# Optimization experiments

Measured on AMD Instinct MI355X. Metric: run time of the kernel, lower is better.

## Reference

```python
import jax, jax.numpy as jnp
import numpy as np

NUM_CLASSES = 2
LOG2_NC = float(np.log2(NUM_CLASSES))


def _conv(x, w, b=None):
    # NCHW conv, stride 1, SAME padding (kernel 3 pad 1 or kernel 1 pad 0)
    y = jax.lax.conv_general_dilated(x, w, (1, 1), 'SAME',
                                     dimension_numbers=('NCHW', 'OIHW', 'NCHW'))
    if b is not None:
        y = y + b[None, :, None, None]
    return y


def _uncertainty_map(ds):
    # entropy over class dim, thresholded to {0,1}
    logp = jax.nn.log_softmax(ds, axis=1)            # [B,C,H,W]
    prob = jnp.exp(logp)
    # torch uses log2(prob + 1e-6); replicate exactly
    ent = -jnp.sum(prob * jnp.log2(prob + 1e-6), axis=1) / LOG2_NC  # [B,H,W]
    return (ent >= 0.001).astype(jnp.float32)


def _unob(tar, amap):
    # vectorized UnoB with S=3: interior pixels with tar!=0 get pro=0 unless
    # 4*tar == sum of the 4-neighborhood (i.e. locally constant label)
    t = tar  # [B,H,W] int
    nb = t[:, 2:, 1:-1] + t[:, :-2, 1:-1] + t[:, 1:-1, 2:] + t[:, 1:-1, :-2]
    center = t[:, 1:-1, 1:-1]
    inner_pro = jnp.where((center != 0) & (4 * center != nb), 0.0, 1.0)
    pro = jnp.ones_like(amap)
    pro = pro.at[:, 1:-1, 1:-1].set(inner_pro)
    return amap * pro


def setup_inputs() -> dict:
    key = jax.random.key(0)
    ks = jax.random.split(key, 6)
    B, C, H, W = 8, 128, 128, 128
    return {
        'x': jax.random.normal(ks[0], (B, C, H, W), jnp.float32),
        'skip': jax.random.normal(ks[1], (B, C, H, W), jnp.float32),
        'tar': jax.random.randint(ks[2], (B, 1, H, W), 0, NUM_CLASSES, jnp.int64)
            if jax.config.jax_enable_x64 else
            jax.random.randint(ks[2], (B, 1, H, W), 0, NUM_CLASSES).astype(jnp.int32),
        'W1': jax.random.normal(ks[3], (128, 256, 3, 3), jnp.float32) * 0.05,
        'b1': jnp.zeros((128,), jnp.float32),
        'W2': jax.random.normal(ks[4], (128, 128, 3, 3), jnp.float32) * 0.05,
        'b2': jnp.zeros((128,), jnp.float32),
        'Wds': jax.random.normal(ks[5], (NUM_CLASSES, 128, 1, 1), jnp.float32) * 0.05,
    }


def reference(x, skip, tar, W1, b1, W2, b2, Wds):
    h = jnp.concatenate([x, skip], axis=1)            # [B,2*dim,H,W]
    h = jax.nn.leaky_relu(_conv(h, W1, b1), 0.01)     # [B,dim,H,W]
    h = jax.nn.leaky_relu(_conv(h, W2, b2), 0.01)
    ds = _conv(h, Wds)                                # [B,num_classes,H,W]
    amap = _uncertainty_map(ds)                       # [B,H,W]
    amap = _unob(tar[:, 0], amap)                     # UnoB refinement, S=3
    return h, ds, amap
```

## Files before the change

### kernel.cpp

```cpp
#include <hip/hip_runtime.h>

typedef float f32x16 __attribute__((ext_vector_type(16)));
typedef short bf16x8 __attribute__((ext_vector_type(8)));
typedef unsigned int u32;

static __device__ __forceinline__ unsigned short f2bf(float f) {
  union { float f; unsigned int u; } v;
  v.f = f;
  return (unsigned short)((v.u + 0x7FFFu + ((v.u >> 16) & 1u)) >> 16);
}

static __device__ __forceinline__ void gl_lds16(const unsigned short* g,
                                                unsigned short* l) {
  __builtin_amdgcn_global_load_lds(
      (const __attribute__((address_space(1))) u32*)g,
      (__attribute__((address_space(3))) u32*)l, 16, 0, 0);
}

#define VMCNT4 asm volatile("s_waitcnt vmcnt(4)" ::: "memory")
#define VMCNT0 asm volatile("s_waitcnt vmcnt(0)" ::: "memory")
#define LGKM0 asm volatile("s_waitcnt lgkmcnt(0)" ::: "memory")
#define BAR __builtin_amdgcn_s_barrier()
#define SCHEDB __builtin_amdgcn_sched_barrier(0)

__global__ __launch_bounds__(256) void convert_weights(
    const float* __restrict__ W1, const float* __restrict__ W2,
    unsigned short* __restrict__ W1b, unsigned short* __restrict__ W2b,
    unsigned short* __restrict__ zp) {
  if (blockIdx.x == 1728) {
    uint4* z = (uint4*)zp;
    z[threadIdx.x] = make_uint4(0, 0, 0, 0);
    z[256 + threadIdx.x] = make_uint4(0, 0, 0, 0);
    return;
  }
  int i = blockIdx.x * 256 + threadIdx.x;
  if (i < 294912) {
    int e = i & 7, co = (i >> 3) & 127, r = i >> 10;
    int tap = r % 9, pc = r / 9;
    int ci = (pc >> 1) * 16 + (pc & 1) * 8 + e;
    W1b[i] = f2bf(W1[(co * 256 + ci) * 9 + tap]);
  } else {
    int j = i - 294912;
    if (j < 147456) {
      int e = j & 7, co = (j >> 3) & 127, r = j >> 10;
      int tap = r % 9, pc = r / 9;
      int ci = (pc >> 1) * 16 + (pc & 1) * 8 + e;
      W2b[j] = f2bf(W2[(co * 128 + ci) * 9 + tap]);
    }
  }
}

__global__ __launch_bounds__(256) void transpose_to_bf16(
    const float* __restrict__ x, const float* __restrict__ skip,
    unsigned short* __restrict__ dst) {
  int bid = blockIdx.x;
  const float* src = (bid < 1024) ? x : skip;
  int cigb = (bid < 1024) ? 0 : 16;
  int row = bid & 1023;
  int b = row >> 7, y = row & 127;
  const float* s = src + (long)b * 128 * 16384 + (long)y * 128;
  for (int it = 0; it < 8; ++it) {
    int u = it * 256 + (int)threadIdx.x;
    int cig = u >> 7, px = u & 127;
    unsigned short pk[8];
#pragma unroll
    for (int e = 0; e < 8; ++e)
      pk[e] = f2bf(s[(long)(cig * 8 + e) * 16384 + px]);
    uint4 vv;
    vv.x = (unsigned)pk[0] | ((unsigned)pk[1] << 16);
    vv.y = (unsigned)pk[2] | ((unsigned)pk[3] << 16);
    vv.z = (unsigned)pk[4] | ((unsigned)pk[5] << 16);
    vv.w = (unsigned)pk[6] | ((unsigned)pk[7] << 16);
    *(uint4*)(&dst[(((long)row * 32 + cigb + cig) * 130 + px + 1) * 8]) = vv;
  }
  if (cigb == 0 && threadIdx.x < 64) {
    int g = threadIdx.x >> 1;
    long col = (threadIdx.x & 1) * 129L;
    *(uint4*)(&dst[(((long)row * 32 + g) * 130 + col) * 8]) = make_uint4(0, 0, 0, 0);
  }
}

template <int CIN, bool FUSE_DS>
__global__ __launch_bounds__(256, 2) void conv3x3(
    const unsigned short* __restrict__ src,
    const unsigned short* __restrict__ wt,
    const float* __restrict__ bias,
    const unsigned short* __restrict__ zp,
    unsigned short* __restrict__ dst_bf16,
    float* __restrict__ dst_f32,
    const float* __restrict__ wds,
    const int* __restrict__ tar,
    float* __restrict__ ds,
    float* __restrict__ amap) {
  constexpr int CPG = CIN / 8;
  constexpr int NC = CIN / 16;
  __shared__ unsigned short in_tile[2][1040 * 8];
  __shared__ float sb[128];
  __shared__ float w0s[128], w1s[128];
  __shared__ float sc[2 * 4 * 2 * 32];

  const int tid = threadIdx.x;
  const int wg = (blockIdx.x & 7) * 64 + (blockIdx.x >> 3);
  const int b = wg >> 6;
  const int y0 = (wg & 63) * 2;
  const int lane = tid & 63, wave = tid >> 6;
  const int wco = wave & 1, wrow = wave >> 1;
  const int l31 = lane & 31, kh = lane >> 5;

  if (tid < 128) {
    sb[tid] = bias[tid];
    if constexpr (FUSE_DS) {
      w0s[tid] = wds[tid];
      w1s[tid] = wds[128 + tid];
    }
  }

#define STAGE_IN(cic, bufi)                                                    \
  {                                                                            \
    _Pragma("unroll") for (int j = 0; j < 4; ++j) {                            \
      int o = wave * 4 + j;                                                    \
      int s = o * 64 + lane;                                                   \
      int p = s >= 520;                                                        \
      int r = s - p * 520;                                                     \
      int hy = r / 130;                                                        \
      int hx = r - hy * 130;                                                   \
      int gy = y0 - 1 + hy;                                                    \
      const unsigned short* g =                                                \
          (gy >= 0 && gy < 128)                                                \
              ? src + ((size_t)((b * 128 + gy) * CPG) + (size_t)(cic)*2 + p) * \
                          1040 +                                               \
                    hx * 8                                                     \
              : zp + lane * 8;                                                 \
      gl_lds16(g, &in_tile[bufi][(size_t)o * 512]);                            \
    }                                                                          \
  }

#define LOAD_TAIL(cic, v)                                                      \
  {                                                                            \
    if (tid < 16) {                                                            \
      int gy_ = y0 + 2;                                                        \
      if (gy_ < 128)                                                           \
        v = *(const uint4*)(src +                                              \
                            ((size_t)((b * 128 + gy_) * CPG) +                 \
                             (size_t)(cic)*2 + 1) *                            \
                                1040 +                                         \
                            (114 + tid) * 8);                                  \
    }                                                                          \
  }

#define WRITE_TAIL(bufi, v)                                                    \
  {                                                                            \
    if (tid < 16) *(uint4*)(&in_tile[bufi][(size_t)(1024 + tid) * 8]) = v;     \
  }

  f32x16 acc[2][4] = {};

  const unsigned short* wlane =
      wt + (size_t)kh * 9216 + (size_t)(wco * 64 + l31) * 8;

  {
    uint4 tv = make_uint4(0, 0, 0, 0);
    LOAD_TAIL(0, tv);
    STAGE_IN(0, 0);
    VMCNT0;
    WRITE_TAIL(0, tv);
    LGKM0;
    BAR;
    SCHEDB;
  }
  bf16x8 a0[3], a1[3];
#pragma unroll
  for (int t = 0; t < 3; ++t) {
    a0[t] = *(const bf16x8*)(wlane + t * 1024);
    a1[t] = *(const bf16x8*)(wlane + t * 1024 + 256);
  }

  for (int cic = 0; cic < NC; ++cic) {
    const int cur = cic & 1, nbuf = cur ^ 1;
    const bool more = (cic + 1 < NC);
    uint4 tl = make_uint4(0, 0, 0, 0);
    SCHEDB;
    if (more) {
      LOAD_TAIL(cic + 1, tl);
      STAGE_IN(cic + 1, nbuf);
      SCHEDB;
      VMCNT4;
      SCHEDB;
      WRITE_TAIL(nbuf, tl);
    } else {
      VMCNT0;
    }
    LGKM0;
    BAR;
    SCHEDB;

    const unsigned short* wl = wlane + (size_t)cic * 18432;
    const unsigned short* wlnext = wlane + (size_t)(more ? cic + 1 : cic) * 18432;
    const unsigned short* it = &in_tile[cur][0];
    const size_t ib = (size_t)kh * 4160;
#pragma unroll
    for (int ky = 0; ky < 3; ++ky) {
      const int hy = ky + wrow;
      bf16x8 n0[3], n1[3];
      if (ky < 2) {
#pragma unroll
        for (int t = 0; t < 3; ++t) {
          n0[t] = *(const bf16x8*)(wl + (ky * 3 + 3 + t) * 1024);
          n1[t] = *(const bf16x8*)(wl + (ky * 3 + 3 + t) * 1024 + 256);
        }
      } else {
#pragma unroll
        for (int t = 0; t < 3; ++t) {
          n0[t] = *(const bf16x8*)(wlnext + t * 1024);
          n1[t] = *(const bf16x8*)(wlnext + t * 1024 + 256);
        }
      }
#pragma unroll
      for (int kx = 0; kx < 3; ++kx) {
        bf16x8 b0 = *(const bf16x8*)(&it[ib + (size_t)(hy * 130 + l31 + kx) * 8]);
        bf16x8 b1 = *(const bf16x8*)(&it[ib + (size_t)(hy * 130 + 32 + l31 + kx) * 8]);
        bf16x8 b2 = *(const bf16x8*)(&it[ib + (size_t)(hy * 130 + 64 + l31 + kx) * 8]);
        bf16x8 b3 = *(const bf16x8*)(&it[ib + (size_t)(hy * 130 + 96 + l31 + kx) * 8]);
        acc[0][0] = __builtin_amdgcn_mfma_f32_32x32x16_bf16(a0[kx], b0, acc[0][0], 0, 0, 0);
        acc[0][1] = __builtin_amdgcn_mfma_f32_32x32x16_bf16(a0[kx], b1, acc[0][1], 0, 0, 0);
        acc[0][2] = __builtin_amdgcn_mfma_f32_32x32x16_bf16(a0[kx], b2, acc[0][2], 0, 0, 0);
        acc[0][3] = __builtin_amdgcn_mfma_f32_32x32x16_bf16(a0[kx], b3, acc[0][3], 0, 0, 0);
        acc[1][0] = __builtin_amdgcn_mfma_f32_32x32x16_bf16(a1[kx], b0, acc[1][0], 0, 0, 0);
        acc[1][1] = __builtin_amdgcn_mfma_f32_32x32x16_bf16(a1[kx], b1, acc[1][1], 0, 0, 0);
        acc[1][2] = __builtin_amdgcn_mfma_f32_32x32x16_bf16(a1[kx], b2, acc[1][2], 0, 0, 0);
        acc[1][3] = __builtin_amdgcn_mfma_f32_32x32x16_bf16(a1[kx], b3, acc[1][3], 0, 0, 0);
      }
#pragma unroll
      for (int t = 0; t < 3; ++t) { a0[t] = n0[t]; a1[t] = n1[t]; }
    }
    SCHEDB;
    LGKM0;
    BAR;
    SCHEDB;
  }

  const int gyo = y0 + wrow;
  float pd[4][2] = {};
#pragma unroll
  for (int fc = 0; fc < 2; ++fc) {
#pragma unroll
    for (int fp = 0; fp < 4; ++fp) {
      const int px = fp * 32 + l31;
      if constexpr (!FUSE_DS) {
#pragma unroll
        for (int rg = 0; rg < 4; ++rg) {
          const int co0 = wco * 64 + fc * 32 + rg * 8 + kh * 4;
          unsigned short pk[4];
#pragma unroll
          for (int q = 0; q < 4; ++q) {
            float v = acc[fc][fp][rg * 4 + q] + sb[co0 + q];
            v = v > 0.f ? v : 0.01f * v;
            pk[q] = f2bf(v);
          }
          uint2 o;
          o.x = (unsigned)pk[0] | ((unsigned)pk[1] << 16);
          o.y = (unsigned)pk[2] | ((unsigned)pk[3] << 16);
          *(uint2*)(&dst_bf16[(((long)(b * 128 + gyo) * 16 + (co0 >> 3)) * 130 + px + 1) * 8 +
                              kh * 4]) = o;
        }
      } else {
#pragma unroll
        for (int rg = 0; rg < 4; ++rg) {
          const int co0 = wco * 64 + fc * 32 + rg * 8 + kh * 4;
          float4 wv0 = *(const float4*)(&w0s[co0]);
          float4 wv1 = *(const float4*)(&w1s[co0]);
#pragma unroll
          for (int q = 0; q < 4; ++q) {
            float v = acc[fc][fp][rg * 4 + q] + sb[co0 + q];
            v = v > 0.f ? v : 0.01f * v;
            dst_f32[((long)(b * 128 + co0 + q) << 14) + (gyo << 7) + px] = v;
            float wq0 = (q == 0) ? wv0.x : (q == 1) ? wv0.y : (q == 2) ? wv0.z : wv0.w;
            float wq1 = (q == 0) ? wv1.x : (q == 1) ? wv1.y : (q == 2) ? wv1.z : wv1.w;
            pd[fp][0] += wq0 * v;
            pd[fp][1] += wq1 * v;
          }
        }
      }
    }
  }

  if constexpr (!FUSE_DS) {
    if (tid < 64) {
      int row = tid >> 5, g = (tid >> 1) & 15;
      long col = (tid & 1) * 129L;
      *(uint4*)(&dst_bf16[(((long)(b * 128 + y0 + row) * 16 + g) * 130 + col) * 8]) =
          make_uint4(0, 0, 0, 0);
    }
  } else {
#pragma unroll
    for (int fp = 0; fp < 4; ++fp)
#pragma unroll
      for (int c = 0; c < 2; ++c)
        pd[fp][c] += __shfl_xor(pd[fp][c], 32, 64);
    if (wco == 1 && kh == 0) {
#pragma unroll
      for (int fp = 0; fp < 4; ++fp)
#pragma unroll
        for (int c = 0; c < 2; ++c)
          sc[((wrow * 4 + fp) * 2 + c) * 32 + l31] = pd[fp][c];
    }
    __syncthreads();
    if (wco == 0 && kh == 0) {
      const int* tb = tar + (long)b * 16384;
#pragma unroll
      for (int fp = 0; fp < 4; ++fp) {
        const int px = fp * 32 + l31;
        float a0f = pd[fp][0] + sc[((wrow * 4 + fp) * 2 + 0) * 32 + l31];
        float a1f = pd[fp][1] + sc[((wrow * 4 + fp) * 2 + 1) * 32 + l31];
        ds[((long)b * 2) * 16384 + (gyo << 7) + px] = a0f;
        ds[((long)b * 2 + 1) * 16384 + (gyo << 7) + px] = a1f;
        float m = fmaxf(a0f, a1f);
        float e0 = expf(a0f - m), e1 = expf(a1f - m);
        float s = e0 + e1;
        float p0f = e0 / s, p1f = e1 / s;
        float ent = -(p0f * log2f(p0f + 1e-6f) + p1f * log2f(p1f + 1e-6f));
        float un = ent >= 0.001f ? 1.f : 0.f;
        float pro = 1.f;
        if (gyo > 0 && gyo < 127 && px > 0 && px < 127) {
          int c = tb[(gyo << 7) + px];
          if (c != 0) {
            int nb2 = tb[((gyo - 1) << 7) + px] + tb[((gyo + 1) << 7) + px] +
                      tb[(gyo << 7) + px - 1] + tb[(gyo << 7) + px + 1];
            if (4 * c != nb2) pro = 0.f;
          }
        }
        amap[((long)(b * 128 + gyo) << 7) + px] = un * pro;
      }
    }
  }
#undef STAGE_IN
#undef LOAD_TAIL
#undef WRITE_TAIL
}

extern "C" void kernel_launch(void* const* d_in, const int* in_sizes, int n_in,
                              void* d_out, int out_size, void* d_ws, size_t ws_size,
                              hipStream_t stream) {
  const float* x    = (const float*)d_in[0];
  const float* skip = (const float*)d_in[1];
  const int*   tar  = (const int*)d_in[2];
  const float* W1   = (const float*)d_in[3];
  const float* b1   = (const float*)d_in[4];
  const float* W2   = (const float*)d_in[5];
  const float* b2   = (const float*)d_in[6];
  const float* Wds  = (const float*)d_in[7];

  float* out_h  = (float*)d_out;
  float* out_ds = out_h + 16777216;
  float* out_am = out_ds + 262144;

  unsigned short* W1b = (unsigned short*)d_ws;
  unsigned short* W2b = W1b + 294912;
  unsigned short* zp  = W2b + 147456;
  unsigned short* h1  = (unsigned short*)((char*)d_ws + (1u << 20));

  unsigned short* h0 = (unsigned short*)d_out;

  convert_weights<<<1729, 256, 0, stream>>>(W1, W2, W1b, W2b, zp);
  transpose_to_bf16<<<2048, 256, 0, stream>>>(x, skip, h0);
  conv3x3<256, false><<<512, 256, 0, stream>>>(h0, W1b, b1, zp, h1, nullptr,
                                               nullptr, nullptr, nullptr, nullptr);
  conv3x3<128, true><<<512, 256, 0, stream>>>(h1, W2b, b2, zp, nullptr, out_h,
                                              Wds, tar, out_ds, out_am);
}
```

Measured before the change: 151.1 us.

## Split conv3x3 work across 8 waves per block with padded LDS rows

Doubles the block size to 512 threads so each wave computes half the pixel columns (2 MFMA tiles per row instead of 4), cutting accumulator registers and raising waves per CU. The LDS input tile row stride is padded to 136, and staging is simplified to precomputed global pointers with per-wave load counts, removing the separate tail load path. Weight register prefetching across ky/channel chunks is dropped in favour of loading weights right before use, which trades fewer registers for possibly more exposed global-load latency.

After: 178.3 us. 18.0% more time.

```diff
diff --git a/kernel.cpp b/kernel.cpp
--- a/kernel.cpp
+++ b/kernel.cpp
@@ -17,7 +17,8 @@
       (__attribute__((address_space(3))) u32*)l, 16, 0, 0);
 }
 
-#define VMCNT4 asm volatile("s_waitcnt vmcnt(4)" ::: "memory")
+#define VMCNT3 asm volatile("s_waitcnt vmcnt(3)" ::: "memory")
+#define VMCNT2 asm volatile("s_waitcnt vmcnt(2)" ::: "memory")
 #define VMCNT0 asm volatile("s_waitcnt vmcnt(0)" ::: "memory")
 #define LGKM0 asm volatile("s_waitcnt lgkmcnt(0)" ::: "memory")
 #define BAR __builtin_amdgcn_s_barrier()
@@ -81,7 +82,7 @@
 }
 
 template <int CIN, bool FUSE_DS>
-__global__ __launch_bounds__(256, 2) void conv3x3(
+__global__ __launch_bounds__(512, 4) void conv3x3(
     const unsigned short* __restrict__ src,
     const unsigned short* __restrict__ wt,
     const float* __restrict__ bias,
@@ -94,17 +95,17 @@
     float* __restrict__ amap) {
   constexpr int CPG = CIN / 8;
   constexpr int NC = CIN / 16;
-  __shared__ unsigned short in_tile[2][1040 * 8];
+  __shared__ unsigned short in_tile[2][1088 * 8];
   __shared__ float sb[128];
   __shared__ float w0s[128], w1s[128];
-  __shared__ float sc[2 * 4 * 2 * 32];
+  __shared__ float sc[2 * 2 * 2 * 2 * 32];
 
   const int tid = threadIdx.x;
   const int wg = (blockIdx.x & 7) * 64 + (blockIdx.x >> 3);
   const int b = wg >> 6;
   const int y0 = (wg & 63) * 2;
   const int lane = tid & 63, wave = tid >> 6;
-  const int wco = wave & 1, wrow = wave >> 1;
+  const int wco = wave & 1, wpx = (wave >> 1) & 1, wrow = wave >> 2;
   const int l31 = lane & 31, kh = lane >> 5;
 
   if (tid < 128) {
@@ -115,123 +116,76 @@
     }
   }
 
-#define STAGE_IN(cic, bufi)                                                    \
-  {                                                                            \
-    _Pragma("unroll") for (int j = 0; j < 4; ++j) {                            \
-      int o = wave * 4 + j;                                                    \
-      int s = o * 64 + lane;                                                   \
-      int p = s >= 520;                                                        \
-      int r = s - p * 520;                                                     \
-      int hy = r / 130;                                                        \
-      int hx = r - hy * 130;                                                   \
-      int gy = y0 - 1 + hy;                                                    \
-      const unsigned short* g =                                                \
-          (gy >= 0 && gy < 128)                                                \
-              ? src + ((size_t)((b * 128 + gy) * CPG) + (size_t)(cic)*2 + p) * \
-                          1040 +                                               \
-                    hx * 8                                                     \
-              : zp + lane * 8;                                                 \
-      gl_lds16(g, &in_tile[bufi][(size_t)o * 512]);                            \
-    }                                                                          \
-  }
-
-#define LOAD_TAIL(cic, v)                                                      \
-  {                                                                            \
-    if (tid < 16) {                                                            \
-      int gy_ = y0 + 2;                                                        \
-      if (gy_ < 128)                                                           \
-        v = *(const uint4*)(src +                                              \
-                            ((size_t)((b * 128 + gy_) * CPG) +                 \
-                             (size_t)(cic)*2 + 1) *                            \
-                                1040 +                                         \
-                            (114 + tid) * 8);                                  \
-    }                                                                          \
-  }
-
-#define WRITE_TAIL(bufi, v)                                                    \
-  {                                                                            \
-    if (tid < 16) *(uint4*)(&in_tile[bufi][(size_t)(1024 + tid) * 8]) = v;     \
-  }
-
-  f32x16 acc[2][4] = {};
+  const int nops = (wave == 0) ? 3 : 2;
+  const unsigned short* gbase[3];
+  int gstr[3];
+  int lofs[3];
+#pragma unroll
+  for (int i = 0; i < 3; ++i) {
+    const int o = (i < 2) ? (wave * 2 + i) : 16;
+    const int s = o * 64 + lane;
+    const int p = s >= 544;
+    const int r = s - p * 544;
+    const int hy = r / 136;
+    const int hx = r - hy * 136;
+    const int gy = y0 - 1 + hy;
+    const bool ok = (hx < 130) && (gy >= 0) && (gy < 128);
+    gbase[i] = ok ? src + ((size_t)((b * 128 + gy) * CPG) + p) * 1040 + hx * 8
+                  : zp + lane * 8;
+    gstr[i] = ok ? 2080 : 0;
+    lofs[i] = o * 512;
+  }
+
+  f32x16 acc[2][2] = {};
+
+#pragma unroll
+  for (int i = 0; i < 3; ++i)
+    if (i < nops) gl_lds16(gbase[i], &in_tile[0][(size_t)lofs[i]]);
+  VMCNT0;
+  BAR;
 
   const unsigned short* wlane =
       wt + (size_t)kh * 9216 + (size_t)(wco * 64 + l31) * 8;
-
-  {
-    uint4 tv = make_uint4(0, 0, 0, 0);
-    LOAD_TAIL(0, tv);
-    STAGE_IN(0, 0);
-    VMCNT0;
-    WRITE_TAIL(0, tv);
-    LGKM0;
-    BAR;
-    SCHEDB;
-  }
-  bf16x8 a0[3], a1[3];
-#pragma unroll
-  for (int t = 0; t < 3; ++t) {
-    a0[t] = *(const bf16x8*)(wlane + t * 1024);
-    a1[t] = *(const bf16x8*)(wlane + t * 1024 + 256);
-  }
 
   for (int cic = 0; cic < NC; ++cic) {
     const int cur = cic & 1, nbuf = cur ^ 1;
     const bool more = (cic + 1 < NC);
-    uint4 tl = make_uint4(0, 0, 0, 0);
-    SCHEDB;
     if (more) {
-      LOAD_TAIL(cic + 1, tl);
-      STAGE_IN(cic + 1, nbuf);
+#pragma unroll
+      for (int i = 0; i < 3; ++i)
+        if (i < nops)
+          gl_lds16(gbase[i] + (size_t)(cic + 1) * gstr[i],
+                   &in_tile[nbuf][(size_t)lofs[i]]);
       SCHEDB;
-      VMCNT4;
-      SCHEDB;
-      WRITE_TAIL(nbuf, tl);
+      if (wave == 0) { VMCNT3; } else { VMCNT2; }
     } else {
       VMCNT0;
     }
-    LGKM0;
+    SCHEDB;
     BAR;
     SCHEDB;
 
     const unsigned short* wl = wlane + (size_t)cic * 18432;
-    const unsigned short* wlnext = wlane + (size_t)(more ? cic + 1 : cic) * 18432;
     const unsigned short* it = &in_tile[cur][0];
-    const size_t ib = (size_t)kh * 4160;
+    const size_t ib = (size_t)kh * (544 * 8);
 #pragma unroll
     for (int ky = 0; ky < 3; ++ky) {
       const int hy = ky + wrow;
-      bf16x8 n0[3], n1[3];
-      if (ky < 2) {
-#pragma unroll
-        for (int t = 0; t < 3; ++t) {
-          n0[t] = *(const bf16x8*)(wl + (ky * 3 + 3 + t) * 1024);
-          n1[t] = *(const bf16x8*)(wl + (ky * 3 + 3 + t) * 1024 + 256);
-        }
-      } else {
-#pragma unroll
-        for (int t = 0; t < 3; ++t) {
-          n0[t] = *(const bf16x8*)(wlnext + t * 1024);
-          n1[t] = *(const bf16x8*)(wlnext + t * 1024 + 256);
-        }
+      bf16x8 a0[3], a1[3];
+#pragma unroll
+      for (int t = 0; t < 3; ++t) {
+        a0[t] = *(const bf16x8*)(wl + (ky * 3 + t) * 1024);
+        a1[t] = *(const bf16x8*)(wl + (ky * 3 + t) * 1024 + 256);
       }
 #pragma unroll
       for (int kx = 0; kx < 3; ++kx) {
-        bf16x8 b0 = *(const bf16x8*)(&it[ib + (size_t)(hy * 130 + l31 + kx) * 8]);
-        bf16x8 b1 = *(const bf16x8*)(&it[ib + (size_t)(hy * 130 + 32 + l31 + kx) * 8]);
-        bf16x8 b2 = *(const bf16x8*)(&it[ib + (size_t)(hy * 130 + 64 + l31 + kx) * 8]);
-        bf16x8 b3 = *(const bf16x8*)(&it[ib + (size_t)(hy * 130 + 96 + l31 + kx) * 8]);
+        bf16x8 b0 = *(const bf16x8*)(&it[ib + (size_t)(hy * 136 + wpx * 64 + l31 + kx) * 8]);
+        bf16x8 b1 = *(const bf16x8*)(&it[ib + (size_t)(hy * 136 + wpx * 64 + 32 + l31 + kx) * 8]);
         acc[0][0] = __builtin_amdgcn_mfma_f32_32x32x16_bf16(a0[kx], b0, acc[0][0], 0, 0, 0);
         acc[0][1] = __builtin_amdgcn_mfma_f32_32x32x16_bf16(a0[kx], b1, acc[0][1], 0, 0, 0);
-        acc[0][2] = __builtin_amdgcn_mfma_f32_32x32x16_bf16(a0[kx], b2, acc[0][2], 0, 0, 0);
-        acc[0][3] = __builtin_amdgcn_mfma_f32_32x32x16_bf16(a0[kx], b3, acc[0][3], 0, 0, 0);
         acc[1][0] = __builtin_amdgcn_mfma_f32_32x32x16_bf16(a1[kx], b0, acc[1][0], 0, 0, 0);
         acc[1][1] = __builtin_amdgcn_mfma_f32_32x32x16_bf16(a1[kx], b1, acc[1][1], 0, 0, 0);
-        acc[1][2] = __builtin_amdgcn_mfma_f32_32x32x16_bf16(a1[kx], b2, acc[1][2], 0, 0, 0);
-        acc[1][3] = __builtin_amdgcn_mfma_f32_32x32x16_bf16(a1[kx], b3, acc[1][3], 0, 0, 0);
       }
-#pragma unroll
-      for (int t = 0; t < 3; ++t) { a0[t] = n0[t]; a1[t] = n1[t]; }
     }
     SCHEDB;
     LGKM0;
@@ -240,12 +194,12 @@
   }
 
   const int gyo = y0 + wrow;
-  float pd[4][2] = {};
+  float pd[2][2] = {};
 #pragma unroll
   for (int fc = 0; fc < 2; ++fc) {
 #pragma unroll
-    for (int fp = 0; fp < 4; ++fp) {
-      const int px = fp * 32 + l31;
+    for (int fp = 0; fp < 2; ++fp) {
+      const int px = wpx * 64 + fp * 32 + l31;
       if constexpr (!FUSE_DS) {
 #pragma unroll
         for (int rg = 0; rg < 4; ++rg) {
@@ -293,25 +247,25 @@
     }
   } else {
 #pragma unroll
-    for (int fp = 0; fp < 4; ++fp)
+    for (int fp = 0; fp < 2; ++fp)
 #pragma unroll
       for (int c = 0; c < 2; ++c)
         pd[fp][c] += __shfl_xor(pd[fp][c], 32, 64);
     if (wco == 1 && kh == 0) {
 #pragma unroll
-      for (int fp = 0; fp < 4; ++fp)
+      for (int fp = 0; fp < 2; ++fp)
 #pragma unroll
         for (int c = 0; c < 2; ++c)
-          sc[((wrow * 4 + fp) * 2 + c) * 32 + l31] = pd[fp][c];
+          sc[((((wrow * 2 + wpx) * 2 + fp) * 2 + c)) * 32 + l31] = pd[fp][c];
     }
     __syncthreads();
     if (wco == 0 && kh == 0) {
       const int* tb = tar + (long)b * 16384;
 #pragma unroll
-      for (int fp = 0; fp < 4; ++fp) {
-        const int px = fp * 32 + l31;
-        float a0f = pd[fp][0] + sc[((wrow * 4 + fp) * 2 + 0) * 32 + l31];
-        float a1f = pd[fp][1] + sc[((wrow * 4 + fp) * 2 + 1) * 32 + l31];
+      for (int fp = 0; fp < 2; ++fp) {
+        const int px = wpx * 64 + fp * 32 + l31;
+        float a0f = pd[fp][0] + sc[((((wrow * 2 + wpx) * 2 + fp) * 2 + 0)) * 32 + l31];
+        float a1f = pd[fp][1] + sc[((((wrow * 2 + wpx) * 2 + fp) * 2 + 1)) * 32 + l31];
         ds[((long)b * 2) * 16384 + (gyo << 7) + px] = a0f;
         ds[((long)b * 2 + 1) * 16384 + (gyo << 7) + px] = a1f;
         float m = fmaxf(a0f, a1f);
@@ -333,9 +287,6 @@
       }
     }
   }
-#undef STAGE_IN
-#undef LOAD_TAIL
-#undef WRITE_TAIL
 }
 
 extern "C" void kernel_launch(void* const* d_in, const int* in_sizes, int n_in,
@@ -363,8 +314,8 @@
 
   convert_weights<<<1729, 256, 0, stream>>>(W1, W2, W1b, W2b, zp);
   transpose_to_bf16<<<2048, 256, 0, stream>>>(x, skip, h0);
-  conv3x3<256, false><<<512, 256, 0, stream>>>(h0, W1b, b1, zp, h1, nullptr,
+  conv3x3<256, false><<<512, 512, 0, stream>>>(h0, W1b, b1, zp, h1, nullptr,
                                                nullptr, nullptr, nullptr, nullptr);
-  conv3x3<128, true><<<512, 256, 0, stream>>>(h1, W2b, b2, zp, nullptr, out_h,
+  conv3x3<128, true><<<512, 512, 0, stream>>>(h1, W2b, b2, zp, nullptr, out_h,
                                               Wds, tar, out_ds, out_am);
 }
```
